# Kernel tuning notes

Hardware: AMD Instinct MI355X
Metric: run time of the kernel (lower is better)

Reference implementation:

```python
import jax, jax.numpy as jnp
import numpy as np

H, D = 16, 64          # num_heads, head_dim
OUT = H * D            # out_dim = 1024
W1, W2 = 32, 32        # sliding windows
EPS_NORM = 1e-7
EPS_LN = 1e-5


def setup_inputs() -> dict:
    key = jax.random.key(0)
    ks = jax.random.split(key, 6)
    B, S, IN = 2, 2048, 1024
    x = jax.random.normal(ks[0], (B, S, IN), dtype=jnp.float32)
    scale = 0.02
    W_Q = jax.random.normal(ks[1], (IN, OUT), dtype=jnp.float32) * scale
    W_K = jax.random.normal(ks[2], (IN, OUT), dtype=jnp.float32) * scale
    W_V = jax.random.normal(ks[3], (IN, OUT), dtype=jnp.float32) * scale
    W_Kp = jax.random.normal(ks[4], (IN, OUT), dtype=jnp.float32) * scale
    W_O = jax.random.normal(ks[5], (OUT, OUT), dtype=jnp.float32) * scale
    ln_gamma = jnp.ones((OUT,), dtype=jnp.float32)
    ln_beta = jnp.zeros((OUT,), dtype=jnp.float32)
    return {"x": x, "W_Q": W_Q, "W_K": W_K, "W_V": W_V, "W_Kp": W_Kp,
            "W_O": W_O, "ln_gamma": ln_gamma, "ln_beta": ln_beta}


def _l2norm(t):
    return t / (jnp.linalg.norm(t, axis=-1, keepdims=True) + EPS_NORM)


def reference(x, W_Q, W_K, W_V, W_Kp, W_O, ln_gamma, ln_beta):
    B, S, _ = x.shape
    # projections -> (B, S, H, D)
    Q = _l2norm((x @ W_Q).reshape(B, S, H, D))
    K = _l2norm((x @ W_K).reshape(B, S, H, D))
    Kp = _l2norm((x @ W_Kp).reshape(B, S, H, D))
    V = (x @ W_V).reshape(B, S, H, D)
    # windowed keys/values (last w1/w2 positions, as in the PyTorch fallback)
    K_win = K[:, -W1:]
    Kp_win = Kp[:, -W2:]
    V_win = V[:, -W1:]
    Vp_win = V[:, -W2:]
    # triple product A_ijk = q.k.k' / sqrt(D) -> (B, S, H, w1, w2)
    A = jnp.einsum('bshd,bjhd,bkhd->bshjk', Q, K_win, Kp_win) / jnp.sqrt(jnp.float32(D))
    # causal window mask: allow j <= i + w1 - S and k <= i + w2 - S
    s_idx = jnp.arange(S)[:, None, None]
    j_idx = jnp.arange(W1)[None, :, None]
    k_idx = jnp.arange(W2)[None, None, :]
    mask = (j_idx > s_idx + (W1 - S)) | (k_idx > s_idx + (W2 - S))  # (S, w1, w2)
    neg_inf = jnp.float32(-jnp.inf)
    A = jnp.where(mask[None, :, None, :, :], neg_inf, A)
    # joint softmax over (j, k); fully-masked query rows produce zeros
    A_flat = A.reshape(B, S, H, W1 * W2)
    all_masked = jnp.all(A_flat == neg_inf, axis=-1, keepdims=True)
    A_safe = jnp.where(all_masked, 0.0, A_flat)
    P = jax.nn.softmax(A_safe, axis=-1)
    P = jnp.where(all_masked, 0.0, P).reshape(B, S, H, W1, W2)
    # value outer-product weighting (V' = V)
    Z = jnp.einsum('bshjk,bjhd,bkhd->bshd', P, V_win, Vp_win)
    out = Z.reshape(B, S, OUT) @ W_O
    out = out + x  # residual (shapes match)
    # LayerNorm
    mu = jnp.mean(out, axis=-1, keepdims=True)
    var = jnp.mean((out - mu) ** 2, axis=-1, keepdims=True)
    out = (out - mu) / jnp.sqrt(var + EPS_LN) * ln_gamma + ln_beta
    return out
```

## Files before the change

kernel.cpp:

```cpp
#include <hip/hip_runtime.h>
#include <math.h>


#define XS 68

#define NSPLIT    8
#define YPART_SZ  262144
#define Z_OFF     (NSPLIT * YPART_SZ)
#define DPART_OFF (Z_OFF + 65536)


__device__ __forceinline__ int sw_idx(int row, int d) {
  return row * 64 + ((((d >> 2) + (row >> 2)) & 15) << 2) + (d & 3);
}

__global__ __launch_bounds__(256, 2) void proj_kernel(
    const float* __restrict__ x,
    const float* __restrict__ Wq, const float* __restrict__ Wk,
    const float* __restrict__ Wkp, const float* __restrict__ Wv,
    float* __restrict__ ws) {
  __shared__ float xs[128 * 65];
  const int tid = threadIdx.x;
  const int z    = blockIdx.x >> 4;
  const int col0 = (blockIdx.x & 15) * 64;
  const int ks   = blockIdx.y;
  const int k0   = ks * 128;
  const float* __restrict__ W =
      (z == 0) ? Wq : ((z == 1) ? Wk : ((z == 2) ? Wkp : Wv));

  #pragma unroll
  for (int i = 0; i < 8; i++) {
    int e = i * 256 + tid;
    int r = e >> 5, q = e & 31;
    int b = r >> 5, t = r & 31;
    float4 v = *(const float4*)(x + ((b * 2048 + 2016 + t) * 1024 + k0 + q * 4));
    xs[(q * 4 + 0) * 65 + r] = v.x;
    xs[(q * 4 + 1) * 65 + r] = v.y;
    xs[(q * 4 + 2) * 65 + r] = v.z;
    xs[(q * 4 + 3) * 65 + r] = v.w;
  }
  __syncthreads();

  const int wave = __builtin_amdgcn_readfirstlane(tid >> 6);
  const int lane = tid & 63;
  const float* __restrict__ Wt = W + (size_t)k0 * 1024 + col0 + wave * 16;

  float acc[16];
  #pragma unroll
  for (int c = 0; c < 16; c++) acc[c] = 0.f;

  #pragma unroll 4
  for (int kk = 0; kk < 128; kk++) {
    float xv = xs[kk * 65 + lane];
    const float* __restrict__ wrow = Wt + kk * 1024;
    #pragma unroll
    for (int c = 0; c < 16; c++) acc[c] = fmaf(xv, wrow[c], acc[c]);
  }

  __syncthreads();
  #pragma unroll
  for (int c = 0; c < 16; c++) xs[lane * 65 + wave * 16 + c] = acc[c];
  __syncthreads();
  float* __restrict__ Yo = ws + (size_t)ks * YPART_SZ + z * 65536 + col0;
  #pragma unroll
  for (int i = 0; i < 16; i++) {
    int r = wave * 16 + i;
    Yo[r * 1024 + lane] = xs[r * 65 + lane];
  }
}

__global__ __launch_bounds__(256) void attn_kernel(
    const float* __restrict__ ws, float* __restrict__ Zout) {
  __shared__ float Kn[32 * 64], Kp[32 * 64];
  __shared__ float Vs[32 * XS];
  __shared__ float Pt[4][32 * 36];
  __shared__ float qs[4][64];
  const int tid = threadIdx.x;
  const int wave = tid >> 6, lane = tid & 63;
  const int h = blockIdx.y, b = blockIdx.z;

  #pragma unroll
  for (int i = 0; i < 8; i++) {
    int e = i * 256 + tid;
    int row = e >> 6, d = e & 63;
    int src = (b * 32 + row) * 1024 + h * 64 + d;
    float kn = 0.f, kp = 0.f, vv = 0.f;
    #pragma unroll
    for (int s = 0; s < NSPLIT; s++) {
      const float* __restrict__ p = ws + (size_t)s * YPART_SZ + src;
      kn += p[65536];
      kp += p[131072];
      vv += p[196608];
    }
    Kn[sw_idx(row, d)] = kn;
    Kp[sw_idx(row, d)] = kp;
    Vs[row * XS + d] = vv;
  }
  __syncthreads();

  for (int rr = 0; rr < 8; rr++) {
    int row = wave * 8 + rr;
    int a = sw_idx(row, lane);
    float kv = Kn[a];
    float s2 = kv * kv;
    #pragma unroll
    for (int off = 1; off < 64; off <<= 1) s2 += __shfl_xor(s2, off);
    Kn[a] = kv * (1.f / (sqrtf(s2) + 1e-7f));
    float pv = Kp[a];
    float p2 = pv * pv;
    #pragma unroll
    for (int off = 1; off < 64; off <<= 1) p2 += __shfl_xor(p2, off);
    Kp[a] = pv * (1.f / (sqrtf(p2) + 1e-7f));
  }
  __syncthreads();

  const int m = blockIdx.x * 4 + wave;
  const int r = b * 32 + m;

  float q = 0.f;
  {
    int src = r * 1024 + h * 64 + lane;
    #pragma unroll
    for (int s = 0; s < NSPLIT; s++) q += ws[(size_t)s * YPART_SZ + src];
  }
  float q2 = q * q;
  #pragma unroll
  for (int off = 1; off < 64; off <<= 1) q2 += __shfl_xor(q2, off);
  q *= (1.f / (sqrtf(q2) + 1e-7f));
  qs[wave][lane] = q;
  __builtin_amdgcn_wave_barrier();

  const int lj = lane >> 3, lk = lane & 7;
  float acc[4][4];
  #pragma unroll
  for (int a = 0; a < 4; a++)
    #pragma unroll
    for (int c = 0; c < 4; c++) acc[a][c] = 0.f;

  const float* qw = qs[wave];
  for (int dq = 0; dq < 16; dq++) {
    float4 q4 = *(const float4*)(qw + dq * 4);
    const int cj = (((dq + lj) & 15) << 2);
    const int ck = (((dq + lk) & 15) << 2);
    float4 t4[4], kp4[4];
    #pragma unroll
    for (int tj = 0; tj < 4; tj++) {
      float4 kv = *(const float4*)(Kn + (lj * 4 + tj) * 64 + cj);
      t4[tj].x = q4.x * kv.x; t4[tj].y = q4.y * kv.y;
      t4[tj].z = q4.z * kv.z; t4[tj].w = q4.w * kv.w;
    }
    #pragma unroll
    for (int tk = 0; tk < 4; tk++)
      kp4[tk] = *(const float4*)(Kp + (lk * 4 + tk) * 64 + ck);
    #pragma unroll
    for (int tj = 0; tj < 4; tj++) {
      #pragma unroll
      for (int tk = 0; tk < 4; tk++) {
        acc[tj][tk] += t4[tj].x * kp4[tk].x + t4[tj].y * kp4[tk].y
                     + t4[tj].z * kp4[tk].z + t4[tj].w * kp4[tk].w;
      }
    }
  }

  float amax = -1e30f;
  #pragma unroll
  for (int tj = 0; tj < 4; tj++)
    #pragma unroll
    for (int tk = 0; tk < 4; tk++) {
      int j = lj * 4 + tj, k = lk * 4 + tk;
      if (j <= m && k <= m) amax = fmaxf(amax, acc[tj][tk] * 0.125f);
    }
  #pragma unroll
  for (int off = 1; off < 64; off <<= 1) amax = fmaxf(amax, __shfl_xor(amax, off));

  float lsum = 0.f;
  float* ptw = Pt[wave];
  #pragma unroll
  for (int tk = 0; tk < 4; tk++) {
    int k = lk * 4 + tk;
    float4 ev;
    float* e = (float*)&ev;
    #pragma unroll
    for (int tj = 0; tj < 4; tj++) {
      int j = lj * 4 + tj;
      float x = 0.f;
      if (j <= m && k <= m) x = __expf(acc[tj][tk] * 0.125f - amax);
      e[tj] = x;
      lsum += x;
    }
    *(float4*)(ptw + k * 36 + lj * 4) = ev;
  }
  #pragma unroll
  for (int off = 1; off < 64; off <<= 1) lsum += __shfl_xor(lsum, off);
  float inv = 1.f / lsum;
  __builtin_amdgcn_wave_barrier();

  float vreg[32];
  #pragma unroll
  for (int k = 0; k < 32; k++) vreg[k] = Vs[k * XS + lane];
  float zacc = 0.f;
  for (int k = 0; k <= m; k++) {
    float g0 = 0.f, g1 = 0.f, g2 = 0.f, g3 = 0.f;
    #pragma unroll
    for (int jq = 0; jq < 8; jq++) {
      float4 p = *(const float4*)(ptw + k * 36 + jq * 4);
      g0 = fmaf(p.x, vreg[jq * 4 + 0], g0);
      g1 = fmaf(p.y, vreg[jq * 4 + 1], g1);
      g2 = fmaf(p.z, vreg[jq * 4 + 2], g2);
      g3 = fmaf(p.w, vreg[jq * 4 + 3], g3);
    }
    zacc = fmaf((g0 + g1) + (g2 + g3), vreg[k], zacc);
  }
  Zout[r * 1024 + h * 64 + lane] = zacc * inv;
}

__global__ __launch_bounds__(256, 2) void wo_kernel(
    const float* __restrict__ Zr, const float* __restrict__ Wo,
    float* __restrict__ ws) {
  __shared__ float xs[128 * 65];
  const int tid = threadIdx.x;
  const int col0 = blockIdx.x * 64;
  const int ks   = blockIdx.y;
  const int k0   = ks * 128;

  #pragma unroll
  for (int i = 0; i < 8; i++) {
    int e = i * 256 + tid;
    int r = e >> 5, q = e & 31;
    float4 v = *(const float4*)(Zr + r * 1024 + k0 + q * 4);
    xs[(q * 4 + 0) * 65 + r] = v.x;
    xs[(q * 4 + 1) * 65 + r] = v.y;
    xs[(q * 4 + 2) * 65 + r] = v.z;
    xs[(q * 4 + 3) * 65 + r] = v.w;
  }
  __syncthreads();

  const int wave = __builtin_amdgcn_readfirstlane(tid >> 6);
  const int lane = tid & 63;
  const float* __restrict__ Wt = Wo + (size_t)k0 * 1024 + col0 + wave * 16;

  float acc[16];
  #pragma unroll
  for (int c = 0; c < 16; c++) acc[c] = 0.f;

  #pragma unroll 4
  for (int kk = 0; kk < 128; kk++) {
    float xv = xs[kk * 65 + lane];
    const float* __restrict__ wrow = Wt + kk * 1024;
    #pragma unroll
    for (int c = 0; c < 16; c++) acc[c] = fmaf(xv, wrow[c], acc[c]);
  }

  __syncthreads();
  #pragma unroll
  for (int c = 0; c < 16; c++) xs[lane * 65 + wave * 16 + c] = acc[c];
  __syncthreads();
  float* __restrict__ Do = ws + (size_t)DPART_OFF + (size_t)ks * 65536 + col0;
  #pragma unroll
  for (int i = 0; i < 16; i++) {
    int r = wave * 16 + i;
    Do[r * 1024 + lane] = xs[r * 65 + lane];
  }
}

__global__ __launch_bounds__(256, 4) void ln_kernel(
    const float4* __restrict__ x4, const float4* __restrict__ dpart4,
    const float4* __restrict__ g4, const float4* __restrict__ b4,
    float4* __restrict__ out4) {
  const int tid = threadIdx.x;
  const int wave = tid >> 6, lane = tid & 63;
  const int row = blockIdx.x * 4 + wave;
  const int b = row >> 11, s = row & 2047;

  float4 v[4];
  #pragma unroll
  for (int i = 0; i < 4; i++) v[i] = x4[row * 256 + i * 64 + lane];
  if (s >= 2016) {
    int drow = b * 32 + (s - 2016);
    #pragma unroll
    for (int i = 0; i < 4; i++) {
      #pragma unroll
      for (int sp = 0; sp < NSPLIT; sp++) {
        float4 d = dpart4[sp * 16384 + drow * 256 + i * 64 + lane];
        v[i].x += d.x; v[i].y += d.y; v[i].z += d.z; v[i].w += d.w;
      }
    }
  }
  float sum = 0.f, ss = 0.f;
  #pragma unroll
  for (int i = 0; i < 4; i++) {
    sum += v[i].x + v[i].y + v[i].z + v[i].w;
    ss  += v[i].x * v[i].x + v[i].y * v[i].y + v[i].z * v[i].z + v[i].w * v[i].w;
  }
  #pragma unroll
  for (int off = 1; off < 64; off <<= 1) {
    sum += __shfl_xor(sum, off);
    ss  += __shfl_xor(ss, off);
  }
  float mu   = sum * (1.f / 1024.f);
  float var  = ss * (1.f / 1024.f) - mu * mu;
  float rstd = rsqrtf(var + 1e-5f);

  #pragma unroll
  for (int i = 0; i < 4; i++) {
    float4 g = g4[i * 64 + lane];
    float4 be = b4[i * 64 + lane];
    float4 o;
    o.x = (v[i].x - mu) * rstd * g.x + be.x;
    o.y = (v[i].y - mu) * rstd * g.y + be.y;
    o.z = (v[i].z - mu) * rstd * g.z + be.z;
    o.w = (v[i].w - mu) * rstd * g.w + be.w;
    out4[row * 256 + i * 64 + lane] = o;
  }
}

extern "C" void kernel_launch(void* const* d_in, const int* in_sizes, int n_in,
                              void* d_out, int out_size, void* d_ws, size_t ws_size,
                              hipStream_t stream) {
  const float* x   = (const float*)d_in[0];
  const float* Wq  = (const float*)d_in[1];
  const float* Wk  = (const float*)d_in[2];
  const float* Wv  = (const float*)d_in[3];
  const float* Wkp = (const float*)d_in[4];
  const float* Wo  = (const float*)d_in[5];
  const float* gam = (const float*)d_in[6];
  const float* bet = (const float*)d_in[7];
  float* out = (float*)d_out;
  float* ws  = (float*)d_ws;

  hipLaunchKernelGGL(proj_kernel, dim3(64, 8), dim3(256), 0, stream,
                     x, Wq, Wk, Wkp, Wv, ws);
  hipLaunchKernelGGL(attn_kernel, dim3(8, 16, 2), dim3(256), 0, stream,
                     ws, ws + Z_OFF);
  hipLaunchKernelGGL(wo_kernel, dim3(16, 8), dim3(256), 0, stream,
                     ws + Z_OFF, Wo, ws);
  hipLaunchKernelGGL(ln_kernel, dim3(1024), dim3(256), 0, stream,
                     (const float4*)x, (const float4*)(ws + DPART_OFF),
                     (const float4*)gam, (const float4*)bet, (float4*)out);
}
```

Baseline: 148.7 us.

## Fuse all stages into one cooperative persistent kernel with grid syncs

Replaces the four separate launches with one cooperative kernel of 1024 blocks that steps through projection, split-K reduction, attention, the W_O product and the windowed LayerNorm, separated by grid.sync. LayerNorm for the non-window rows now runs alongside the projection blocks. The split-K partial sums are reduced once into a full buffer instead of being re-summed inside every attention block. Attention is also spread over 512 blocks with two active waves each. The aim is to cut launch gaps and overlap independent work, at the cost of grid barrier overhead and a requirement that all blocks be co-resident. A five-kernel fallback path runs if the cooperative launch fails.

```diff
diff --git a/kernel.cpp b/kernel.cpp
--- a/kernel.cpp
+++ b/kernel.cpp
@@ -1,37 +1,42 @@
 #include <hip/hip_runtime.h>
+#include <hip/hip_cooperative_groups.h>
 #include <math.h>
 
-
-#define XS 68
-
-#define NSPLIT    8
-#define YPART_SZ  262144
-#define Z_OFF     (NSPLIT * YPART_SZ)
-#define DPART_OFF (Z_OFF + 65536)
-
+namespace cg = cooperative_groups;
+
+
+#define NS 8
+#define YPART_OFF 0
+#define YFULL_OFF 2097152
+#define ZOFF      2359296
+#define DPART_OFF 2424832
+
+#define YQ  0
+#define YK  65536
+#define YKP 131072
+#define YV  196608
+
+#define SMEM_FLOATS 8576
 
 __device__ __forceinline__ int sw_idx(int row, int d) {
   return row * 64 + ((((d >> 2) + (row >> 2)) & 15) << 2) + (d & 3);
 }
 
-__global__ __launch_bounds__(256, 2) void proj_kernel(
-    const float* __restrict__ x,
+__device__ __forceinline__ void proj_tile(
+    int pid, int tid, const float* __restrict__ x,
     const float* __restrict__ Wq, const float* __restrict__ Wk,
     const float* __restrict__ Wkp, const float* __restrict__ Wv,
-    float* __restrict__ ws) {
-  __shared__ float xs[128 * 65];
-  const int tid = threadIdx.x;
-  const int z    = blockIdx.x >> 4;
-  const int col0 = (blockIdx.x & 15) * 64;
-  const int ks   = blockIdx.y;
+    float* __restrict__ ws, float* xs) {
+  const int z    = (pid & 63) >> 4;
+  const int col0 = (pid & 15) * 64;
+  const int ks   = pid >> 6;
   const int k0   = ks * 128;
   const float* __restrict__ W =
       (z == 0) ? Wq : ((z == 1) ? Wk : ((z == 2) ? Wkp : Wv));
 
   #pragma unroll
   for (int i = 0; i < 8; i++) {
-    int e = i * 256 + tid;
-    int r = e >> 5, q = e & 31;
+    int e = i * 256 + tid; int r = e >> 5, q = e & 31;
     int b = r >> 5, t = r & 31;
     float4 v = *(const float4*)(x + ((b * 2048 + 2016 + t) * 1024 + k0 + q * 4));
     xs[(q * 4 + 0) * 65 + r] = v.x;
@@ -44,11 +49,9 @@
   const int wave = __builtin_amdgcn_readfirstlane(tid >> 6);
   const int lane = tid & 63;
   const float* __restrict__ Wt = W + (size_t)k0 * 1024 + col0 + wave * 16;
-
   float acc[16];
   #pragma unroll
   for (int c = 0; c < 16; c++) acc[c] = 0.f;
-
   #pragma unroll 4
   for (int kk = 0; kk < 128; kk++) {
     float xv = xs[kk * 65 + lane];
@@ -56,12 +59,11 @@
     #pragma unroll
     for (int c = 0; c < 16; c++) acc[c] = fmaf(xv, wrow[c], acc[c]);
   }
-
   __syncthreads();
   #pragma unroll
   for (int c = 0; c < 16; c++) xs[lane * 65 + wave * 16 + c] = acc[c];
   __syncthreads();
-  float* __restrict__ Yo = ws + (size_t)ks * YPART_SZ + z * 65536 + col0;
+  float* __restrict__ Yo = ws + YPART_OFF + (size_t)ks * 262144 + z * 65536 + col0;
   #pragma unroll
   for (int i = 0; i < 16; i++) {
     int r = wave * 16 + i;
@@ -69,218 +71,20 @@
   }
 }
 
-__global__ __launch_bounds__(256) void attn_kernel(
-    const float* __restrict__ ws, float* __restrict__ Zout) {
-  __shared__ float Kn[32 * 64], Kp[32 * 64];
-  __shared__ float Vs[32 * XS];
-  __shared__ float Pt[4][32 * 36];
-  __shared__ float qs[4][64];
-  const int tid = threadIdx.x;
-  const int wave = tid >> 6, lane = tid & 63;
-  const int h = blockIdx.y, b = blockIdx.z;
-
-  #pragma unroll
-  for (int i = 0; i < 8; i++) {
-    int e = i * 256 + tid;
-    int row = e >> 6, d = e & 63;
-    int src = (b * 32 + row) * 1024 + h * 64 + d;
-    float kn = 0.f, kp = 0.f, vv = 0.f;
-    #pragma unroll
-    for (int s = 0; s < NSPLIT; s++) {
-      const float* __restrict__ p = ws + (size_t)s * YPART_SZ + src;
-      kn += p[65536];
-      kp += p[131072];
-      vv += p[196608];
-    }
-    Kn[sw_idx(row, d)] = kn;
-    Kp[sw_idx(row, d)] = kp;
-    Vs[row * XS + d] = vv;
-  }
-  __syncthreads();
-
-  for (int rr = 0; rr < 8; rr++) {
-    int row = wave * 8 + rr;
-    int a = sw_idx(row, lane);
-    float kv = Kn[a];
-    float s2 = kv * kv;
-    #pragma unroll
-    for (int off = 1; off < 64; off <<= 1) s2 += __shfl_xor(s2, off);
-    Kn[a] = kv * (1.f / (sqrtf(s2) + 1e-7f));
-    float pv = Kp[a];
-    float p2 = pv * pv;
-    #pragma unroll
-    for (int off = 1; off < 64; off <<= 1) p2 += __shfl_xor(p2, off);
-    Kp[a] = pv * (1.f / (sqrtf(p2) + 1e-7f));
-  }
-  __syncthreads();
-
-  const int m = blockIdx.x * 4 + wave;
-  const int r = b * 32 + m;
-
-  float q = 0.f;
-  {
-    int src = r * 1024 + h * 64 + lane;
-    #pragma unroll
-    for (int s = 0; s < NSPLIT; s++) q += ws[(size_t)s * YPART_SZ + src];
-  }
-  float q2 = q * q;
-  #pragma unroll
-  for (int off = 1; off < 64; off <<= 1) q2 += __shfl_xor(q2, off);
-  q *= (1.f / (sqrtf(q2) + 1e-7f));
-  qs[wave][lane] = q;
-  __builtin_amdgcn_wave_barrier();
-
-  const int lj = lane >> 3, lk = lane & 7;
-  float acc[4][4];
-  #pragma unroll
-  for (int a = 0; a < 4; a++)
-    #pragma unroll
-    for (int c = 0; c < 4; c++) acc[a][c] = 0.f;
-
-  const float* qw = qs[wave];
-  for (int dq = 0; dq < 16; dq++) {
-    float4 q4 = *(const float4*)(qw + dq * 4);
-    const int cj = (((dq + lj) & 15) << 2);
-    const int ck = (((dq + lk) & 15) << 2);
-    float4 t4[4], kp4[4];
-    #pragma unroll
-    for (int tj = 0; tj < 4; tj++) {
-      float4 kv = *(const float4*)(Kn + (lj * 4 + tj) * 64 + cj);
-      t4[tj].x = q4.x * kv.x; t4[tj].y = q4.y * kv.y;
-      t4[tj].z = q4.z * kv.z; t4[tj].w = q4.w * kv.w;
-    }
-    #pragma unroll
-    for (int tk = 0; tk < 4; tk++)
-      kp4[tk] = *(const float4*)(Kp + (lk * 4 + tk) * 64 + ck);
-    #pragma unroll
-    for (int tj = 0; tj < 4; tj++) {
-      #pragma unroll
-      for (int tk = 0; tk < 4; tk++) {
-        acc[tj][tk] += t4[tj].x * kp4[tk].x + t4[tj].y * kp4[tk].y
-                     + t4[tj].z * kp4[tk].z + t4[tj].w * kp4[tk].w;
-      }
-    }
-  }
-
-  float amax = -1e30f;
-  #pragma unroll
-  for (int tj = 0; tj < 4; tj++)
-    #pragma unroll
-    for (int tk = 0; tk < 4; tk++) {
-      int j = lj * 4 + tj, k = lk * 4 + tk;
-      if (j <= m && k <= m) amax = fmaxf(amax, acc[tj][tk] * 0.125f);
-    }
-  #pragma unroll
-  for (int off = 1; off < 64; off <<= 1) amax = fmaxf(amax, __shfl_xor(amax, off));
-
-  float lsum = 0.f;
-  float* ptw = Pt[wave];
-  #pragma unroll
-  for (int tk = 0; tk < 4; tk++) {
-    int k = lk * 4 + tk;
-    float4 ev;
-    float* e = (float*)&ev;
-    #pragma unroll
-    for (int tj = 0; tj < 4; tj++) {
-      int j = lj * 4 + tj;
-      float x = 0.f;
-      if (j <= m && k <= m) x = __expf(acc[tj][tk] * 0.125f - amax);
-      e[tj] = x;
-      lsum += x;
-    }
-    *(float4*)(ptw + k * 36 + lj * 4) = ev;
-  }
-  #pragma unroll
-  for (int off = 1; off < 64; off <<= 1) lsum += __shfl_xor(lsum, off);
-  float inv = 1.f / lsum;
-  __builtin_amdgcn_wave_barrier();
-
-  float vreg[32];
-  #pragma unroll
-  for (int k = 0; k < 32; k++) vreg[k] = Vs[k * XS + lane];
-  float zacc = 0.f;
-  for (int k = 0; k <= m; k++) {
-    float g0 = 0.f, g1 = 0.f, g2 = 0.f, g3 = 0.f;
-    #pragma unroll
-    for (int jq = 0; jq < 8; jq++) {
-      float4 p = *(const float4*)(ptw + k * 36 + jq * 4);
-      g0 = fmaf(p.x, vreg[jq * 4 + 0], g0);
-      g1 = fmaf(p.y, vreg[jq * 4 + 1], g1);
-      g2 = fmaf(p.z, vreg[jq * 4 + 2], g2);
-      g3 = fmaf(p.w, vreg[jq * 4 + 3], g3);
-    }
-    zacc = fmaf((g0 + g1) + (g2 + g3), vreg[k], zacc);
-  }
-  Zout[r * 1024 + h * 64 + lane] = zacc * inv;
-}
-
-__global__ __launch_bounds__(256, 2) void wo_kernel(
-    const float* __restrict__ Zr, const float* __restrict__ Wo,
-    float* __restrict__ ws) {
-  __shared__ float xs[128 * 65];
-  const int tid = threadIdx.x;
-  const int col0 = blockIdx.x * 64;
-  const int ks   = blockIdx.y;
-  const int k0   = ks * 128;
-
-  #pragma unroll
-  for (int i = 0; i < 8; i++) {
-    int e = i * 256 + tid;
-    int r = e >> 5, q = e & 31;
-    float4 v = *(const float4*)(Zr + r * 1024 + k0 + q * 4);
-    xs[(q * 4 + 0) * 65 + r] = v.x;
-    xs[(q * 4 + 1) * 65 + r] = v.y;
-    xs[(q * 4 + 2) * 65 + r] = v.z;
-    xs[(q * 4 + 3) * 65 + r] = v.w;
-  }
-  __syncthreads();
-
-  const int wave = __builtin_amdgcn_readfirstlane(tid >> 6);
-  const int lane = tid & 63;
-  const float* __restrict__ Wt = Wo + (size_t)k0 * 1024 + col0 + wave * 16;
-
-  float acc[16];
-  #pragma unroll
-  for (int c = 0; c < 16; c++) acc[c] = 0.f;
-
-  #pragma unroll 4
-  for (int kk = 0; kk < 128; kk++) {
-    float xv = xs[kk * 65 + lane];
-    const float* __restrict__ wrow = Wt + kk * 1024;
-    #pragma unroll
-    for (int c = 0; c < 16; c++) acc[c] = fmaf(xv, wrow[c], acc[c]);
-  }
-
-  __syncthreads();
-  #pragma unroll
-  for (int c = 0; c < 16; c++) xs[lane * 65 + wave * 16 + c] = acc[c];
-  __syncthreads();
-  float* __restrict__ Do = ws + (size_t)DPART_OFF + (size_t)ks * 65536 + col0;
-  #pragma unroll
-  for (int i = 0; i < 16; i++) {
-    int r = wave * 16 + i;
-    Do[r * 1024 + lane] = xs[r * 65 + lane];
-  }
-}
-
-__global__ __launch_bounds__(256, 4) void ln_kernel(
+template <bool WIN>
+__device__ __forceinline__ void ln_row(
+    int row, int drow, int lane,
     const float4* __restrict__ x4, const float4* __restrict__ dpart4,
     const float4* __restrict__ g4, const float4* __restrict__ b4,
     float4* __restrict__ out4) {
-  const int tid = threadIdx.x;
-  const int wave = tid >> 6, lane = tid & 63;
-  const int row = blockIdx.x * 4 + wave;
-  const int b = row >> 11, s = row & 2047;
-
   float4 v[4];
   #pragma unroll
   for (int i = 0; i < 4; i++) v[i] = x4[row * 256 + i * 64 + lane];
-  if (s >= 2016) {
-    int drow = b * 32 + (s - 2016);
+  if (WIN) {
     #pragma unroll
     for (int i = 0; i < 4; i++) {
       #pragma unroll
-      for (int sp = 0; sp < NSPLIT; sp++) {
+      for (int sp = 0; sp < NS; sp++) {
         float4 d = dpart4[sp * 16384 + drow * 256 + i * 64 + lane];
         v[i].x += d.x; v[i].y += d.y; v[i].z += d.z; v[i].w += d.w;
       }
@@ -300,7 +104,6 @@
   float mu   = sum * (1.f / 1024.f);
   float var  = ss * (1.f / 1024.f) - mu * mu;
   float rstd = rsqrtf(var + 1e-5f);
-
   #pragma unroll
   for (int i = 0; i < 4; i++) {
     float4 g = g4[i * 64 + lane];
@@ -312,6 +115,288 @@
     o.w = (v[i].w - mu) * rstd * g.w + be.w;
     out4[row * 256 + i * 64 + lane] = o;
   }
+}
+
+__device__ __forceinline__ void attn_block(
+    int bid, int tid, const float* __restrict__ Yf, float* __restrict__ Z,
+    float* smem) {
+  float* Kn = smem;
+  float* Kp = smem + 2048;
+  float* Vs = smem + 4096;
+  float* qs = smem + 6144;
+  float* Pt = smem + 6272;
+  const int wave = tid >> 6, lane = tid & 63;
+  const int b = bid >> 8, h = (bid >> 4) & 15, sg = bid & 15;
+
+  #pragma unroll
+  for (int i = 0; i < 8; i++) {
+    int e = i * 256 + tid; int row = e >> 6, d = e & 63;
+    int src = (b * 32 + row) * 1024 + h * 64 + d;
+    Kn[sw_idx(row, d)] = Yf[YK + src];
+    Kp[sw_idx(row, d)] = Yf[YKP + src];
+    Vs[row * 64 + d]   = Yf[YV + src];
+  }
+  __syncthreads();
+
+  for (int rr = 0; rr < 8; rr++) {
+    int row = wave * 8 + rr;
+    int a = sw_idx(row, lane);
+    float kv = Kn[a]; float s2 = kv * kv;
+    #pragma unroll
+    for (int off = 1; off < 64; off <<= 1) s2 += __shfl_xor(s2, off);
+    Kn[a] = kv * (1.f / (sqrtf(s2) + 1e-7f));
+    float pv = Kp[a]; float p2 = pv * pv;
+    #pragma unroll
+    for (int off = 1; off < 64; off <<= 1) p2 += __shfl_xor(p2, off);
+    Kp[a] = pv * (1.f / (sqrtf(p2) + 1e-7f));
+  }
+
+  const int m = sg * 2 + wave;
+  const int r = b * 32 + m;
+  if (wave < 2) {
+    float q = Yf[YQ + r * 1024 + h * 64 + lane];
+    float q2 = q * q;
+    #pragma unroll
+    for (int off = 1; off < 64; off <<= 1) q2 += __shfl_xor(q2, off);
+    qs[wave * 64 + lane] = q * (1.f / (sqrtf(q2) + 1e-7f));
+  }
+  __syncthreads();
+
+  if (wave >= 2) return;
+
+  const int lj = lane >> 3, lk = lane & 7;
+  float acc[4][4];
+  #pragma unroll
+  for (int a = 0; a < 4; a++)
+    #pragma unroll
+    for (int c = 0; c < 4; c++) acc[a][c] = 0.f;
+
+  const float* qw = qs + wave * 64;
+  for (int dq = 0; dq < 16; dq++) {
+    float4 q4 = *(const float4*)(qw + dq * 4);
+    const int cj = (((dq + lj) & 15) << 2);
+    const int ck = (((dq + lk) & 15) << 2);
+    float4 t4[4], kp4[4];
+    #pragma unroll
+    for (int tj = 0; tj < 4; tj++) {
+      float4 kv = *(const float4*)(Kn + (lj * 4 + tj) * 64 + cj);
+      t4[tj].x = q4.x * kv.x; t4[tj].y = q4.y * kv.y;
+      t4[tj].z = q4.z * kv.z; t4[tj].w = q4.w * kv.w;
+    }
+    #pragma unroll
+    for (int tk = 0; tk < 4; tk++)
+      kp4[tk] = *(const float4*)(Kp + (lk * 4 + tk) * 64 + ck);
+    #pragma unroll
+    for (int tj = 0; tj < 4; tj++)
+      #pragma unroll
+      for (int tk = 0; tk < 4; tk++)
+        acc[tj][tk] += t4[tj].x * kp4[tk].x + t4[tj].y * kp4[tk].y
+                     + t4[tj].z * kp4[tk].z + t4[tj].w * kp4[tk].w;
+  }
+
+  float amax = -1e30f;
+  #pragma unroll
+  for (int tj = 0; tj < 4; tj++)
+    #pragma unroll
+    for (int tk = 0; tk < 4; tk++) {
+      int j = lj * 4 + tj, k = lk * 4 + tk;
+      if (j <= m && k <= m) amax = fmaxf(amax, acc[tj][tk] * 0.125f);
+    }
+  #pragma unroll
+  for (int off = 1; off < 64; off <<= 1) amax = fmaxf(amax, __shfl_xor(amax, off));
+
+  float lsum = 0.f;
+  float* ptw = Pt + wave * 1152;
+  #pragma unroll
+  for (int tk = 0; tk < 4; tk++) {
+    int k = lk * 4 + tk;
+    float4 ev; float* e = (float*)&ev;
+    #pragma unroll
+    for (int tj = 0; tj < 4; tj++) {
+      int j = lj * 4 + tj;
+      float xv = 0.f;
+      if (j <= m && k <= m) xv = __expf(acc[tj][tk] * 0.125f - amax);
+      e[tj] = xv; lsum += xv;
+    }
+    *(float4*)(ptw + k * 36 + lj * 4) = ev;
+  }
+  #pragma unroll
+  for (int off = 1; off < 64; off <<= 1) lsum += __shfl_xor(lsum, off);
+  float inv = 1.f / lsum;
+  __builtin_amdgcn_wave_barrier();
+
+  float vreg[32];
+  #pragma unroll
+  for (int k = 0; k < 32; k++) vreg[k] = Vs[k * 64 + lane];
+  float zacc = 0.f;
+  for (int k = 0; k <= m; k++) {
+    float g0 = 0.f, g1 = 0.f, g2 = 0.f, g3 = 0.f;
+    #pragma unroll
+    for (int jq = 0; jq < 8; jq++) {
+      float4 p = *(const float4*)(ptw + k * 36 + jq * 4);
+      g0 = fmaf(p.x, vreg[jq * 4 + 0], g0);
+      g1 = fmaf(p.y, vreg[jq * 4 + 1], g1);
+      g2 = fmaf(p.z, vreg[jq * 4 + 2], g2);
+      g3 = fmaf(p.w, vreg[jq * 4 + 3], g3);
+    }
+    zacc = fmaf((g0 + g1) + (g2 + g3), vreg[k], zacc);
+  }
+  Z[r * 1024 + h * 64 + lane] = zacc * inv;
+}
+
+__device__ __forceinline__ void wo_tile(
+    int pid, int tid, const float* __restrict__ Zr,
+    const float* __restrict__ Wo, float* __restrict__ ws, float* xs) {
+  const int col0 = (pid & 15) * 64;
+  const int ks   = pid >> 4;
+  const int k0   = ks * 128;
+  #pragma unroll
+  for (int i = 0; i < 8; i++) {
+    int e = i * 256 + tid; int r = e >> 5, q = e & 31;
+    float4 v = *(const float4*)(Zr + r * 1024 + k0 + q * 4);
+    xs[(q * 4 + 0) * 65 + r] = v.x;
+    xs[(q * 4 + 1) * 65 + r] = v.y;
+    xs[(q * 4 + 2) * 65 + r] = v.z;
+    xs[(q * 4 + 3) * 65 + r] = v.w;
+  }
+  __syncthreads();
+  const int wave = __builtin_amdgcn_readfirstlane(tid >> 6);
+  const int lane = tid & 63;
+  const float* __restrict__ Wt = Wo + (size_t)k0 * 1024 + col0 + wave * 16;
+  float acc[16];
+  #pragma unroll
+  for (int c = 0; c < 16; c++) acc[c] = 0.f;
+  #pragma unroll 4
+  for (int kk = 0; kk < 128; kk++) {
+    float xv = xs[kk * 65 + lane];
+    const float* __restrict__ wrow = Wt + kk * 1024;
+    #pragma unroll
+    for (int c = 0; c < 16; c++) acc[c] = fmaf(xv, wrow[c], acc[c]);
+  }
+  __syncthreads();
+  #pragma unroll
+  for (int c = 0; c < 16; c++) xs[lane * 65 + wave * 16 + c] = acc[c];
+  __syncthreads();
+  float* __restrict__ Do = ws + DPART_OFF + (size_t)ks * 65536 + col0;
+  #pragma unroll
+  for (int i = 0; i < 16; i++) {
+    int r = wave * 16 + i;
+    Do[r * 1024 + lane] = xs[r * 65 + lane];
+  }
+}
+
+__device__ __forceinline__ void reduce_chunk(int bid, int tid,
+                                             float* __restrict__ ws) {
+  int i = bid * 256 + tid;
+  const float4* __restrict__ p4 = (const float4*)(ws + YPART_OFF);
+  float4 a = p4[i];
+  #pragma unroll
+  for (int s = 1; s < NS; s++) {
+    float4 p = p4[(size_t)s * 65536 + i];
+    a.x += p.x; a.y += p.y; a.z += p.z; a.w += p.w;
+  }
+  ((float4*)(ws + YFULL_OFF))[i] = a;
+}
+
+__global__ __launch_bounds__(256, 4) void fused_kernel(
+    const float* __restrict__ x,
+    const float* __restrict__ Wq, const float* __restrict__ Wk,
+    const float* __restrict__ Wkp, const float* __restrict__ Wv,
+    const float* __restrict__ Wo,
+    const float* __restrict__ gam, const float* __restrict__ bet,
+    float* __restrict__ out, float* __restrict__ ws) {
+  cg::grid_group grid = cg::this_grid();
+  __shared__ float smem[SMEM_FLOATS];
+  const int tid = threadIdx.x, bid = blockIdx.x;
+  const int wave = tid >> 6, lane = tid & 63;
+  const float4* x4 = (const float4*)x;
+  const float4* g4 = (const float4*)gam;
+  const float4* b4 = (const float4*)bet;
+  float4* out4 = (float4*)out;
+
+  if (bid < 512) {
+    proj_tile(bid, tid, x, Wq, Wk, Wkp, Wv, ws, smem);
+  } else {
+    int base = (bid - 512) * 8 + wave * 2;
+    #pragma unroll
+    for (int i = 0; i < 2; i++) {
+      int rid = base + i;
+      if (rid < 4032) {
+        int b = rid >= 2016 ? 1 : 0;
+        int s = rid - b * 2016;
+        ln_row<false>(b * 2048 + s, 0, lane, x4, nullptr, g4, b4, out4);
+      }
+    }
+  }
+  grid.sync();
+
+  if (bid < 256) reduce_chunk(bid, tid, ws);
+  grid.sync();
+
+  if (bid < 512) attn_block(bid, tid, ws + YFULL_OFF, ws + ZOFF, smem);
+  grid.sync();
+
+  if (bid < 128) wo_tile(bid, tid, ws + ZOFF, Wo, ws, smem);
+  grid.sync();
+
+  if (bid < 16) {
+    int rid = bid * 4 + wave;
+    int b = rid >> 5, sl = rid & 31;
+    ln_row<true>(b * 2048 + 2016 + sl, rid, lane, x4,
+                 (const float4*)(ws + DPART_OFF), g4, b4, out4);
+  }
+}
+
+__global__ __launch_bounds__(256, 4) void k_p1(
+    const float* __restrict__ x,
+    const float* __restrict__ Wq, const float* __restrict__ Wk,
+    const float* __restrict__ Wkp, const float* __restrict__ Wv,
+    const float* __restrict__ gam, const float* __restrict__ bet,
+    float* __restrict__ out, float* __restrict__ ws) {
+  __shared__ float smem[SMEM_FLOATS];
+  const int tid = threadIdx.x, bid = blockIdx.x;
+  const int wave = tid >> 6, lane = tid & 63;
+  if (bid < 512) {
+    proj_tile(bid, tid, x, Wq, Wk, Wkp, Wv, ws, smem);
+  } else {
+    int base = (bid - 512) * 8 + wave * 2;
+    #pragma unroll
+    for (int i = 0; i < 2; i++) {
+      int rid = base + i;
+      if (rid < 4032) {
+        int b = rid >= 2016 ? 1 : 0;
+        int s = rid - b * 2016;
+        ln_row<false>(b * 2048 + s, 0, lane, (const float4*)x, nullptr,
+                      (const float4*)gam, (const float4*)bet, (float4*)out);
+      }
+    }
+  }
+}
+
+__global__ __launch_bounds__(256, 4) void k_p2(float* __restrict__ ws) {
+  reduce_chunk(blockIdx.x, threadIdx.x, ws);
+}
+
+__global__ __launch_bounds__(256, 4) void k_p3(float* __restrict__ ws) {
+  __shared__ float smem[SMEM_FLOATS];
+  attn_block(blockIdx.x, threadIdx.x, ws + YFULL_OFF, ws + ZOFF, smem);
+}
+
+__global__ __launch_bounds__(256, 4) void k_p4(const float* __restrict__ Wo,
+                                               float* __restrict__ ws) {
+  __shared__ float smem[SMEM_FLOATS];
+  wo_tile(blockIdx.x, threadIdx.x, ws + ZOFF, Wo, ws, smem);
+}
+
+__global__ __launch_bounds__(256, 4) void k_p5(
+    const float* __restrict__ x, const float* __restrict__ gam,
+    const float* __restrict__ bet, float* __restrict__ out,
+    float* __restrict__ ws) {
+  int rid = blockIdx.x * 4 + (threadIdx.x >> 6);
+  int b = rid >> 5, sl = rid & 31;
+  ln_row<true>(b * 2048 + 2016 + sl, rid, threadIdx.x & 63, (const float4*)x,
+               (const float4*)(ws + DPART_OFF), (const float4*)gam,
+               (const float4*)bet, (float4*)out);
 }
 
 extern "C" void kernel_launch(void* const* d_in, const int* in_sizes, int n_in,
@@ -328,13 +413,17 @@
   float* out = (float*)d_out;
   float* ws  = (float*)d_ws;
 
-  hipLaunchKernelGGL(proj_kernel, dim3(64, 8), dim3(256), 0, stream,
-                     x, Wq, Wk, Wkp, Wv, ws);
-  hipLaunchKernelGGL(attn_kernel, dim3(8, 16, 2), dim3(256), 0, stream,
-                     ws, ws + Z_OFF);
-  hipLaunchKernelGGL(wo_kernel, dim3(16, 8), dim3(256), 0, stream,
-                     ws + Z_OFF, Wo, ws);
-  hipLaunchKernelGGL(ln_kernel, dim3(1024), dim3(256), 0, stream,
-                     (const float4*)x, (const float4*)(ws + DPART_OFF),
-                     (const float4*)gam, (const float4*)bet, (float4*)out);
-}
+  void* args[] = { (void*)&x, (void*)&Wq, (void*)&Wk, (void*)&Wkp, (void*)&Wv,
+                   (void*)&Wo, (void*)&gam, (void*)&bet, (void*)&out, (void*)&ws };
+  hipError_t err = hipLaunchCooperativeKernel(
+      (const void*)fused_kernel, dim3(1024), dim3(256), args, 0, stream);
+  if (err != hipSuccess) {
+    hipLaunchKernelGGL(k_p1, dim3(1024), dim3(256), 0, stream,
+                       x, Wq, Wk, Wkp, Wv, gam, bet, out, ws);
+    hipLaunchKernelGGL(k_p2, dim3(256), dim3(256), 0, stream, ws);
+    hipLaunchKernelGGL(k_p3, dim3(512), dim3(256), 0, stream, ws);
+    hipLaunchKernelGGL(k_p4, dim3(128), dim3(256), 0, stream, Wo, ws);
+    hipLaunchKernelGGL(k_p5, dim3(16), dim3(256), 0, stream,
+                       x, gam, bet, out, ws);
+  }
+}
```

New measurement: 590.4 us. 3.97x slower.
